# Kernel tuning notes

Measured on AMD Instinct MI355X. Metric: run time of the kernel, lower is better.

## Reference

```python
import jax, jax.numpy as jnp
import numpy as np

IN_F = 4096
OUT_F = 4096
BITS = 8
EPS = 1e-5
BATCH, SEQ = 4, 2048


def setup_inputs() -> dict:
    key = jax.random.key(0)
    k1, k2, k3 = jax.random.split(key, 3)
    bound = 1.0 / np.sqrt(IN_F)
    x = jax.random.normal(k1, (BATCH, SEQ, IN_F), dtype=jnp.float32)
    weight = jax.random.uniform(k2, (OUT_F, IN_F), dtype=jnp.float32, minval=-bound, maxval=bound)
    bias = jax.random.uniform(k3, (OUT_F,), dtype=jnp.float32, minval=-bound, maxval=bound)
    return {"x": x, "weight": weight, "bias": bias}


def _ste_round_clip(v, lo, hi):
    # round+clip with straight-through estimator
    q = jnp.clip(jnp.round(v), lo, hi)
    return v + jax.lax.stop_gradient(q - v)


def reference(x, weight, bias):
    q = jnp.float32(2 ** (BITS - 1))  # 128 for int8
    # weight ternarization: absmean scale, round to {-1,0,1}
    w_scale = jnp.maximum(jnp.mean(jnp.abs(weight)), EPS)
    w_q = _ste_round_clip(weight / w_scale, -1.0, 1.0)  # ternary [O,I]
    # activation int8 quantization: absmax scale over whole tensor (dim=None)
    gamma = jnp.maximum(jnp.max(jnp.abs(x)), EPS)
    x_q = _ste_round_clip(x * (q / gamma), -q, q - 1.0)  # int8 range values
    # integer-domain matmul then dequantize
    out = jnp.einsum('bsi,oi->bso', x_q, w_q) * (gamma * w_scale / q)
    return out + bias
```

## Files before the change

kernel.cpp:

```cpp
#include <hip/hip_runtime.h>
#include <stdint.h>

#define GLOBAL_AS __attribute__((address_space(1)))
#define LDS_AS __attribute__((address_space(3)))

typedef int v4i  __attribute__((ext_vector_type(4)));
typedef int v16i __attribute__((ext_vector_type(16)));

static constexpr int M = 8192;
static constexpr int N = 4096;
static constexpr int K = 4096;
static constexpr float F_EPS = 1e-5f;


__global__ void reduce_kernel(const float4* __restrict__ x, const float4* __restrict__ w,
                              float* __restrict__ pmax, double* __restrict__ psum) {
    const int b = blockIdx.x;
    const int t = threadIdx.x;
    if (b < 1024) {
        float m = 0.f;
        const int n4 = M * K / 4;
        for (int i = b * 256 + t; i < n4; i += 1024 * 256) {
            float4 v = x[i];
            m = fmaxf(m, fmaxf(fmaxf(fabsf(v.x), fabsf(v.y)), fmaxf(fabsf(v.z), fabsf(v.w))));
        }
#pragma unroll
        for (int off = 32; off > 0; off >>= 1) m = fmaxf(m, __shfl_down(m, off, 64));
        __shared__ float red[4];
        if ((t & 63) == 0) red[t >> 6] = m;
        __syncthreads();
        if (t == 0) pmax[b] = fmaxf(fmaxf(red[0], red[1]), fmaxf(red[2], red[3]));
    } else {
        double s = 0.0;
        const int n4 = N * K / 4;
        for (int i = (b - 1024) * 256 + t; i < n4; i += 512 * 256) {
            float4 v = w[i];
            s += (double)fabsf(v.x);
            s += (double)fabsf(v.y);
            s += (double)fabsf(v.z);
            s += (double)fabsf(v.w);
        }
#pragma unroll
        for (int off = 32; off > 0; off >>= 1) s += __shfl_down(s, off, 64);
        __shared__ double dred[4];
        if ((t & 63) == 0) dred[t >> 6] = s;
        __syncthreads();
        if (t == 0) psum[b - 1024] = dred[0] + dred[1] + dred[2] + dred[3];
    }
}

__global__ void finalize_kernel(float* __restrict__ wssc, const float* __restrict__ pmax,
                                const double* __restrict__ psum) {
    const int t = threadIdx.x;
    float m = 0.f;
    for (int i = t; i < 1024; i += 256) m = fmaxf(m, pmax[i]);
#pragma unroll
    for (int off = 32; off > 0; off >>= 1) m = fmaxf(m, __shfl_down(m, off, 64));
    double s = psum[t] + psum[t + 256];
#pragma unroll
    for (int off = 32; off > 0; off >>= 1) s += __shfl_down(s, off, 64);
    __shared__ float red[4];
    __shared__ double dred[4];
    if ((t & 63) == 0) { red[t >> 6] = m; dred[t >> 6] = s; }
    __syncthreads();
    if (t == 0) {
        float gamma = fmaxf(fmaxf(fmaxf(red[0], red[1]), fmaxf(red[2], red[3])), F_EPS);
        double sum = dred[0] + dred[1] + dred[2] + dred[3];
        float wscale = (float)fmax(sum * (1.0 / ((double)N * (double)K)), (double)F_EPS);
        wssc[0] = 128.f / gamma;
        wssc[1] = wscale;
        wssc[2] = gamma * wscale / 128.f;
    }
}

__global__ void quant_kernel(const float4* __restrict__ x, const float4* __restrict__ w,
                             int* __restrict__ xq, int* __restrict__ wq,
                             const float* __restrict__ wssc) {
    const int b = blockIdx.x;
    const int t = threadIdx.x;
    if (b < 2048) {
        const float s = wssc[0];
        const int n4 = M * K / 4;
        for (int i = b * 256 + t; i < n4; i += 2048 * 256) {
            float4 v = x[i];
            int q0 = min(127, max(-128, (int)rintf(v.x * s)));
            int q1 = min(127, max(-128, (int)rintf(v.y * s)));
            int q2 = min(127, max(-128, (int)rintf(v.z * s)));
            int q3 = min(127, max(-128, (int)rintf(v.w * s)));
            xq[i] = (q0 & 255) | ((q1 & 255) << 8) | ((q2 & 255) << 16) | (q3 << 24);
        }
    } else {
        const float ws = wssc[1];
        const int n4 = N * K / 4;
        for (int i = (b - 2048) * 256 + t; i < n4; i += 1024 * 256) {
            float4 v = w[i];
            int q0 = min(1, max(-1, (int)rintf(v.x / ws)));
            int q1 = min(1, max(-1, (int)rintf(v.y / ws)));
            int q2 = min(1, max(-1, (int)rintf(v.z / ws)));
            int q3 = min(1, max(-1, (int)rintf(v.w / ws)));
            wq[i] = (q0 & 255) | ((q1 & 255) << 8) | ((q2 & 255) << 16) | (q3 << 24);
        }
    }
}

__global__ __launch_bounds__(256, 1) void gemm_kernel(
    const int8_t* __restrict__ xq, const int8_t* __restrict__ wq,
    const float* __restrict__ bias, const float* __restrict__ wssc,
    float* __restrict__ out) {

    __shared__ __align__(16) int8_t As0[256 * 64];
    __shared__ __align__(16) int8_t As1[256 * 64];
    __shared__ __align__(16) int8_t Bs0[256 * 64];
    __shared__ __align__(16) int8_t Bs1[256 * 64];

    const int t = threadIdx.x;
    const int lane = t & 63;
    const int wv = t >> 6;
    const int half = lane >> 5;
    const int lr = lane & 31;
    const int wrow0 = (wv >> 1) * 128;
    const int wcol0 = (wv & 1) * 128;
    const int m0 = blockIdx.x * 256;
    const int n0 = blockIdx.y * 256;

    const GLOBAL_AS int8_t* aSrc[4];
    const GLOBAL_AS int8_t* bSrc[4];
    int sLds[4];
#pragma unroll
    for (int j = 0; j < 4; ++j) {
        int idx = j * 256 + t;
        int c = idx >> 6;
        int s = idx & 63;
        int k = s >> 4;
        int rho = ((s & 15) - 4 * k) & 15;
        int row = c * 16 + rho;
        aSrc[j] = (const GLOBAL_AS int8_t*)(xq + (size_t)(m0 + row) * K + k * 16);
        bSrc[j] = (const GLOBAL_AS int8_t*)(wq + (size_t)(n0 + row) * K + k * 16);
        sLds[j] = idx * 16;
    }

    int aOff[2][4], bOff[2][4];
#pragma unroll
    for (int ks = 0; ks < 2; ++ks) {
        int k = ks * 2 + half;
#pragma unroll
        for (int q = 0; q < 4; ++q) {
            int ra = wrow0 + q * 32 + lr;
            aOff[ks][q] = (ra >> 4) * 1024 + k * 256 + (((ra & 15) + 4 * k) & 15) * 16;
            int rb = wcol0 + q * 32 + lr;
            bOff[ks][q] = (rb >> 4) * 1024 + k * 256 + (((rb & 15) + 4 * k) & 15) * 16;
        }
    }

    v16i acc[4][4];
#pragma unroll
    for (int mt = 0; mt < 4; ++mt)
#pragma unroll
        for (int nt = 0; nt < 4; ++nt)
#pragma unroll
            for (int e = 0; e < 16; ++e) acc[mt][nt][e] = 0;

    auto stage = [&](int kt, int8_t* A, int8_t* B) {
#pragma unroll
        for (int j = 0; j < 4; ++j) {
            __builtin_amdgcn_global_load_lds((const GLOBAL_AS void*)(aSrc[j] + kt),
                                             (LDS_AS void*)(A + sLds[j]), 16, 0, 0);
            __builtin_amdgcn_global_load_lds((const GLOBAL_AS void*)(bSrc[j] + kt),
                                             (LDS_AS void*)(B + sLds[j]), 16, 0, 0);
        }
    };

    auto compute = [&](const int8_t* A, const int8_t* B) {
#pragma unroll
        for (int ks = 0; ks < 2; ++ks) {
            v4i a[4], b[4];
#pragma unroll
            for (int q = 0; q < 4; ++q) a[q] = *(const v4i*)(A + aOff[ks][q]);
#pragma unroll
            for (int q = 0; q < 4; ++q) b[q] = *(const v4i*)(B + bOff[ks][q]);
#pragma unroll
            for (int mt = 0; mt < 4; ++mt)
#pragma unroll
                for (int nt = 0; nt < 4; ++nt)
                    acc[mt][nt] = __builtin_amdgcn_mfma_i32_32x32x32_i8(a[mt], b[nt], acc[mt][nt], 0, 0, 0);
        }
    };

    constexpr int NIT = K / 64;
    stage(0, As0, Bs0);
    __syncthreads();
#pragma unroll 1
    for (int it = 0; it < NIT - 2; it += 2) {
        stage((it + 1) * 64, As1, Bs1);
        compute(As0, Bs0);
        __syncthreads();
        stage((it + 2) * 64, As0, Bs0);
        compute(As1, Bs1);
        __syncthreads();
    }
    stage((NIT - 1) * 64, As1, Bs1);
    compute(As0, Bs0);
    __syncthreads();
    compute(As1, Bs1);

    const float scale = wssc[2];
#pragma unroll
    for (int nt = 0; nt < 4; ++nt) {
        int col = n0 + wcol0 + nt * 32 + lr;
        float bv = bias[col];
#pragma unroll
        for (int mt = 0; mt < 4; ++mt) {
            int rb = m0 + wrow0 + mt * 32 + 4 * half;
#pragma unroll
            for (int reg = 0; reg < 16; ++reg) {
                int row = rb + (reg & 3) + 8 * (reg >> 2);
                out[(size_t)row * N + col] = (float)acc[mt][nt][reg] * scale + bv;
            }
        }
    }
}

extern "C" void kernel_launch(void* const* d_in, const int* in_sizes, int n_in,
                              void* d_out, int out_size, void* d_ws, size_t ws_size,
                              hipStream_t stream) {
    const float* x = (const float*)d_in[0];
    const float* w = (const float*)d_in[1];
    const float* bias = (const float*)d_in[2];
    float* out = (float*)d_out;

    float* wssc = (float*)d_ws;
    float* pmax = (float*)((char*)d_ws + 256);
    double* psum = (double*)((char*)d_ws + 4352);
    int8_t* xq = (int8_t*)d_ws + 16384;
    int8_t* wq = xq + (size_t)M * K;

    hipLaunchKernelGGL(reduce_kernel, dim3(1536), dim3(256), 0, stream,
                       (const float4*)x, (const float4*)w, pmax, psum);
    hipLaunchKernelGGL(finalize_kernel, dim3(1), dim3(256), 0, stream, wssc, pmax, psum);
    hipLaunchKernelGGL(quant_kernel, dim3(3072), dim3(256), 0, stream,
                       (const float4*)x, (const float4*)w, (int*)xq, (int*)wq, wssc);
    hipLaunchKernelGGL(gemm_kernel, dim3(M / 256, N / 256), dim3(256), 0, stream,
                       xq, wq, bias, wssc, out);
}
```

Before: 516.1 us.

## Halve GEMM M-tile to 128 for two blocks per CU, unroll pre-passes

The GEMM block tile shrinks from 256x256 to 128x256, each wave now holding a 64x128 sub-tile, with launch bounds raised to two blocks per CU. This halves accumulator registers and A-tile LDS so two workgroups can share a CU and hide latency, at the cost of more B reloads from global memory per output element. The reduce and quantize kernels now process two float4 per thread per iteration, the reduce grid is doubled, and finalize reads the larger partial arrays. The loop bound `i + 256 < n4` is exact only because the sizes divide evenly.

```diff
diff --git a/kernel.cpp b/kernel.cpp
--- a/kernel.cpp
+++ b/kernel.cpp
@@ -17,12 +17,15 @@
                               float* __restrict__ pmax, double* __restrict__ psum) {
     const int b = blockIdx.x;
     const int t = threadIdx.x;
-    if (b < 1024) {
+    if (b < 2048) {
         float m = 0.f;
         const int n4 = M * K / 4;
-        for (int i = b * 256 + t; i < n4; i += 1024 * 256) {
-            float4 v = x[i];
-            m = fmaxf(m, fmaxf(fmaxf(fabsf(v.x), fabsf(v.y)), fmaxf(fabsf(v.z), fabsf(v.w))));
+        int i = b * 512 + t;
+        for (; i + 256 < n4; i += 2048 * 512) {
+            float4 v0 = x[i];
+            float4 v1 = x[i + 256];
+            m = fmaxf(m, fmaxf(fmaxf(fabsf(v0.x), fabsf(v0.y)), fmaxf(fabsf(v0.z), fabsf(v0.w))));
+            m = fmaxf(m, fmaxf(fmaxf(fabsf(v1.x), fabsf(v1.y)), fmaxf(fabsf(v1.z), fabsf(v1.w))));
         }
 #pragma unroll
         for (int off = 32; off > 0; off >>= 1) m = fmaxf(m, __shfl_down(m, off, 64));
@@ -33,19 +36,19 @@
     } else {
         double s = 0.0;
         const int n4 = N * K / 4;
-        for (int i = (b - 1024) * 256 + t; i < n4; i += 512 * 256) {
-            float4 v = w[i];
-            s += (double)fabsf(v.x);
-            s += (double)fabsf(v.y);
-            s += (double)fabsf(v.z);
-            s += (double)fabsf(v.w);
+        int i = (b - 2048) * 512 + t;
+        for (; i + 256 < n4; i += 1024 * 512) {
+            float4 v0 = w[i];
+            float4 v1 = w[i + 256];
+            s += (double)fabsf(v0.x) + (double)fabsf(v0.y) + (double)fabsf(v0.z) + (double)fabsf(v0.w);
+            s += (double)fabsf(v1.x) + (double)fabsf(v1.y) + (double)fabsf(v1.z) + (double)fabsf(v1.w);
         }
 #pragma unroll
         for (int off = 32; off > 0; off >>= 1) s += __shfl_down(s, off, 64);
         __shared__ double dred[4];
         if ((t & 63) == 0) dred[t >> 6] = s;
         __syncthreads();
-        if (t == 0) psum[b - 1024] = dred[0] + dred[1] + dred[2] + dred[3];
+        if (t == 0) psum[b - 2048] = dred[0] + dred[1] + dred[2] + dred[3];
     }
 }
 
@@ -53,10 +56,11 @@
                                 const double* __restrict__ psum) {
     const int t = threadIdx.x;
     float m = 0.f;
-    for (int i = t; i < 1024; i += 256) m = fmaxf(m, pmax[i]);
+#pragma unroll
+    for (int j = 0; j < 8; ++j) m = fmaxf(m, pmax[t + j * 256]);
 #pragma unroll
     for (int off = 32; off > 0; off >>= 1) m = fmaxf(m, __shfl_down(m, off, 64));
-    double s = psum[t] + psum[t + 256];
+    double s = psum[t] + psum[t + 256] + psum[t + 512] + psum[t + 768];
 #pragma unroll
     for (int off = 32; off > 0; off >>= 1) s += __shfl_down(s, off, 64);
     __shared__ float red[4];
@@ -81,35 +85,49 @@
     if (b < 2048) {
         const float s = wssc[0];
         const int n4 = M * K / 4;
-        for (int i = b * 256 + t; i < n4; i += 2048 * 256) {
-            float4 v = x[i];
-            int q0 = min(127, max(-128, (int)rintf(v.x * s)));
-            int q1 = min(127, max(-128, (int)rintf(v.y * s)));
-            int q2 = min(127, max(-128, (int)rintf(v.z * s)));
-            int q3 = min(127, max(-128, (int)rintf(v.w * s)));
-            xq[i] = (q0 & 255) | ((q1 & 255) << 8) | ((q2 & 255) << 16) | (q3 << 24);
+        int i = b * 512 + t;
+        for (; i + 256 < n4; i += 2048 * 512) {
+            float4 v0 = x[i];
+            float4 v1 = x[i + 256];
+            int a0 = min(127, max(-128, (int)rintf(v0.x * s)));
+            int a1 = min(127, max(-128, (int)rintf(v0.y * s)));
+            int a2 = min(127, max(-128, (int)rintf(v0.z * s)));
+            int a3 = min(127, max(-128, (int)rintf(v0.w * s)));
+            xq[i] = (a0 & 255) | ((a1 & 255) << 8) | ((a2 & 255) << 16) | (a3 << 24);
+            int b0 = min(127, max(-128, (int)rintf(v1.x * s)));
+            int b1 = min(127, max(-128, (int)rintf(v1.y * s)));
+            int b2 = min(127, max(-128, (int)rintf(v1.z * s)));
+            int b3 = min(127, max(-128, (int)rintf(v1.w * s)));
+            xq[i + 256] = (b0 & 255) | ((b1 & 255) << 8) | ((b2 & 255) << 16) | (b3 << 24);
         }
     } else {
         const float ws = wssc[1];
         const int n4 = N * K / 4;
-        for (int i = (b - 2048) * 256 + t; i < n4; i += 1024 * 256) {
-            float4 v = w[i];
-            int q0 = min(1, max(-1, (int)rintf(v.x / ws)));
-            int q1 = min(1, max(-1, (int)rintf(v.y / ws)));
-            int q2 = min(1, max(-1, (int)rintf(v.z / ws)));
-            int q3 = min(1, max(-1, (int)rintf(v.w / ws)));
-            wq[i] = (q0 & 255) | ((q1 & 255) << 8) | ((q2 & 255) << 16) | (q3 << 24);
-        }
-    }
-}
-
-__global__ __launch_bounds__(256, 1) void gemm_kernel(
+        int i = (b - 2048) * 512 + t;
+        for (; i + 256 < n4; i += 1024 * 512) {
+            float4 v0 = w[i];
+            float4 v1 = w[i + 256];
+            int a0 = min(1, max(-1, (int)rintf(v0.x / ws)));
+            int a1 = min(1, max(-1, (int)rintf(v0.y / ws)));
+            int a2 = min(1, max(-1, (int)rintf(v0.z / ws)));
+            int a3 = min(1, max(-1, (int)rintf(v0.w / ws)));
+            wq[i] = (a0 & 255) | ((a1 & 255) << 8) | ((a2 & 255) << 16) | (a3 << 24);
+            int b0 = min(1, max(-1, (int)rintf(v1.x / ws)));
+            int b1 = min(1, max(-1, (int)rintf(v1.y / ws)));
+            int b2 = min(1, max(-1, (int)rintf(v1.z / ws)));
+            int b3 = min(1, max(-1, (int)rintf(v1.w / ws)));
+            wq[i + 256] = (b0 & 255) | ((b1 & 255) << 8) | ((b2 & 255) << 16) | (b3 << 24);
+        }
+    }
+}
+
+__global__ __launch_bounds__(256, 2) void gemm_kernel(
     const int8_t* __restrict__ xq, const int8_t* __restrict__ wq,
     const float* __restrict__ bias, const float* __restrict__ wssc,
     float* __restrict__ out) {
 
-    __shared__ __align__(16) int8_t As0[256 * 64];
-    __shared__ __align__(16) int8_t As1[256 * 64];
+    __shared__ __align__(16) int8_t As0[128 * 64];
+    __shared__ __align__(16) int8_t As1[128 * 64];
     __shared__ __align__(16) int8_t Bs0[256 * 64];
     __shared__ __align__(16) int8_t Bs1[256 * 64];
 
@@ -118,14 +136,25 @@
     const int wv = t >> 6;
     const int half = lane >> 5;
     const int lr = lane & 31;
-    const int wrow0 = (wv >> 1) * 128;
-    const int wcol0 = (wv & 1) * 128;
-    const int m0 = blockIdx.x * 256;
+    const int wm0 = (wv >> 1) * 64;
+    const int wn0 = (wv & 1) * 128;
+    const int m0 = blockIdx.x * 128;
     const int n0 = blockIdx.y * 256;
 
-    const GLOBAL_AS int8_t* aSrc[4];
+    const GLOBAL_AS int8_t* aSrc[2];
     const GLOBAL_AS int8_t* bSrc[4];
-    int sLds[4];
+    int aLds[2], bLds[4];
+#pragma unroll
+    for (int j = 0; j < 2; ++j) {
+        int idx = j * 256 + t;
+        int c = idx >> 6;
+        int s = idx & 63;
+        int k = s >> 4;
+        int rho = ((s & 15) - 4 * k) & 15;
+        int row = c * 16 + rho;
+        aSrc[j] = (const GLOBAL_AS int8_t*)(xq + (size_t)(m0 + row) * K + k * 16);
+        aLds[j] = idx * 16;
+    }
 #pragma unroll
     for (int j = 0; j < 4; ++j) {
         int idx = j * 256 + t;
@@ -134,27 +163,29 @@
         int k = s >> 4;
         int rho = ((s & 15) - 4 * k) & 15;
         int row = c * 16 + rho;
-        aSrc[j] = (const GLOBAL_AS int8_t*)(xq + (size_t)(m0 + row) * K + k * 16);
         bSrc[j] = (const GLOBAL_AS int8_t*)(wq + (size_t)(n0 + row) * K + k * 16);
-        sLds[j] = idx * 16;
-    }
-
-    int aOff[2][4], bOff[2][4];
+        bLds[j] = idx * 16;
+    }
+
+    int aOff[2][2], bOff[2][4];
 #pragma unroll
     for (int ks = 0; ks < 2; ++ks) {
         int k = ks * 2 + half;
 #pragma unroll
+        for (int q = 0; q < 2; ++q) {
+            int r = wm0 + q * 32 + lr;
+            aOff[ks][q] = (r >> 4) * 1024 + k * 256 + (((r & 15) + 4 * k) & 15) * 16;
+        }
+#pragma unroll
         for (int q = 0; q < 4; ++q) {
-            int ra = wrow0 + q * 32 + lr;
-            aOff[ks][q] = (ra >> 4) * 1024 + k * 256 + (((ra & 15) + 4 * k) & 15) * 16;
-            int rb = wcol0 + q * 32 + lr;
-            bOff[ks][q] = (rb >> 4) * 1024 + k * 256 + (((rb & 15) + 4 * k) & 15) * 16;
-        }
-    }
-
-    v16i acc[4][4];
-#pragma unroll
-    for (int mt = 0; mt < 4; ++mt)
+            int r = wn0 + q * 32 + lr;
+            bOff[ks][q] = (r >> 4) * 1024 + k * 256 + (((r & 15) + 4 * k) & 15) * 16;
+        }
+    }
+
+    v16i acc[2][4];
+#pragma unroll
+    for (int mt = 0; mt < 2; ++mt)
 #pragma unroll
         for (int nt = 0; nt < 4; ++nt)
 #pragma unroll
@@ -162,24 +193,25 @@
 
     auto stage = [&](int kt, int8_t* A, int8_t* B) {
 #pragma unroll
-        for (int j = 0; j < 4; ++j) {
+        for (int j = 0; j < 2; ++j)
             __builtin_amdgcn_global_load_lds((const GLOBAL_AS void*)(aSrc[j] + kt),
-                                             (LDS_AS void*)(A + sLds[j]), 16, 0, 0);
+                                             (LDS_AS void*)(A + aLds[j]), 16, 0, 0);
+#pragma unroll
+        for (int j = 0; j < 4; ++j)
             __builtin_amdgcn_global_load_lds((const GLOBAL_AS void*)(bSrc[j] + kt),
-                                             (LDS_AS void*)(B + sLds[j]), 16, 0, 0);
-        }
+                                             (LDS_AS void*)(B + bLds[j]), 16, 0, 0);
     };
 
     auto compute = [&](const int8_t* A, const int8_t* B) {
 #pragma unroll
         for (int ks = 0; ks < 2; ++ks) {
-            v4i a[4], b[4];
-#pragma unroll
-            for (int q = 0; q < 4; ++q) a[q] = *(const v4i*)(A + aOff[ks][q]);
+            v4i a[2], b[4];
+#pragma unroll
+            for (int q = 0; q < 2; ++q) a[q] = *(const v4i*)(A + aOff[ks][q]);
 #pragma unroll
             for (int q = 0; q < 4; ++q) b[q] = *(const v4i*)(B + bOff[ks][q]);
 #pragma unroll
-            for (int mt = 0; mt < 4; ++mt)
+            for (int mt = 0; mt < 2; ++mt)
 #pragma unroll
                 for (int nt = 0; nt < 4; ++nt)
                     acc[mt][nt] = __builtin_amdgcn_mfma_i32_32x32x32_i8(a[mt], b[nt], acc[mt][nt], 0, 0, 0);
@@ -206,11 +238,11 @@
     const float scale = wssc[2];
 #pragma unroll
     for (int nt = 0; nt < 4; ++nt) {
-        int col = n0 + wcol0 + nt * 32 + lr;
+        int col = n0 + wn0 + nt * 32 + lr;
         float bv = bias[col];
 #pragma unroll
-        for (int mt = 0; mt < 4; ++mt) {
-            int rb = m0 + wrow0 + mt * 32 + 4 * half;
+        for (int mt = 0; mt < 2; ++mt) {
+            int rb = m0 + wm0 + mt * 32 + 4 * half;
 #pragma unroll
             for (int reg = 0; reg < 16; ++reg) {
                 int row = rb + (reg & 3) + 8 * (reg >> 2);
@@ -230,15 +262,15 @@
 
     float* wssc = (float*)d_ws;
     float* pmax = (float*)((char*)d_ws + 256);
-    double* psum = (double*)((char*)d_ws + 4352);
-    int8_t* xq = (int8_t*)d_ws + 16384;
+    double* psum = (double*)((char*)d_ws + 8448);
+    int8_t* xq = (int8_t*)d_ws + 16640;
     int8_t* wq = xq + (size_t)M * K;
 
-    hipLaunchKernelGGL(reduce_kernel, dim3(1536), dim3(256), 0, stream,
+    hipLaunchKernelGGL(reduce_kernel, dim3(3072), dim3(256), 0, stream,
                        (const float4*)x, (const float4*)w, pmax, psum);
     hipLaunchKernelGGL(finalize_kernel, dim3(1), dim3(256), 0, stream, wssc, pmax, psum);
     hipLaunchKernelGGL(quant_kernel, dim3(3072), dim3(256), 0, stream,
                        (const float4*)x, (const float4*)w, (int*)xq, (int*)wq, wssc);
-    hipLaunchKernelGGL(gemm_kernel, dim3(M / 256, N / 256), dim3(256), 0, stream,
+    hipLaunchKernelGGL(gemm_kernel, dim3(M / 128, N / 256), dim3(256), 0, stream,
                        xq, wq, bias, wssc, out);
 }
```

Measured after the change: 489.5 us. 1.05x faster.
